# Performance work log

Measured on AMD Instinct MI355X. Metric: run time of the kernel, lower is better.

Reference implementation:

```python
import jax, jax.numpy as jnp
import numpy as np

N = 40000      # nodes
E = 640000     # edges (avg degree 16)
IN_DIM = 128
OUT_DIM = 128
HEADS = 4
NEG_SLOPE = 0.01  # torch F.leaky_relu default


def lrelu(x):
    return jnp.where(x >= 0, x, NEG_SLOPE * x)


def gat_layer(h, fc_W, attn_W, edge_w, m_w, src, dst, pd):
    """One GATLayer: z = lrelu(fc(h)); per-edge score; segment softmax over dst; weighted sum.
    fc_W: [D_out, D_in], attn_W: [1, 2*D_out], edge_w/m_w: [1,1] scalars, pd: [E,1]."""
    n = h.shape[0]
    z = lrelu(h @ fc_W.T)                      # [N, D]
    d = z.shape[1]
    # attn_fc(cat(z_src, z_dst)) = z_src@a_l + z_dst@a_r  (no bias)
    a_src = z @ attn_W[0, :d]                  # [N]
    a_dst = z @ attn_W[0, d:]                  # [N]
    a = a_src[src] + a_dst[dst]                # [E]
    ev = pd[:, 0] * edge_w[0, 0]               # edge_fc (Linear(1,1), no bias)
    e = lrelu(a * ev)                          # [E]
    ne = e * m_w[0, 0]                         # m_fc (Linear(1,1), no bias)
    # segment softmax over destination node (DGL mailbox softmax)
    m = jax.ops.segment_max(ne, dst, num_segments=n)
    m = jnp.where(jnp.isfinite(m), m, 0.0)     # empty mailboxes -> 0
    ex = jnp.exp(ne - m[dst])                  # [E]
    s = jax.ops.segment_sum(ex, dst, num_segments=n)
    denom = jnp.where(s > 0, s, 1.0)
    alpha = ex / denom[dst]                    # [E]
    # h_i = sum_j alpha_ij * z_j  (scatter-add over dst)
    return jax.ops.segment_sum(alpha[:, None] * z[src], dst, num_segments=n)


def gru_cell(x, hprev, Wih, Whh, bih, bhh):
    """torch.nn.GRUCell math. Wih/Whh: [3H, H]; gate order: reset, update, new."""
    gi = x @ Wih.T + bih
    gh = hprev @ Whh.T + bhh
    ir, iz, in_ = jnp.split(gi, 3, axis=1)
    hr, hz, hn = jnp.split(gh, 3, axis=1)
    r = jax.nn.sigmoid(ir + hr)
    zg = jax.nn.sigmoid(iz + hz)
    ng = jnp.tanh(in_ + r * hn)
    return (1.0 - zg) * ng + zg * hprev


def setup_inputs() -> dict:
    key = jax.random.key(0)
    ks = jax.random.split(key, 16)
    sc = 0.05
    inp = {
        "h": jax.random.normal(ks[0], (N, IN_DIM), jnp.float32),
        "pd": jax.random.uniform(ks[1], (E, 1), jnp.float32),
        "src": jax.random.randint(ks[2], (E,), 0, N, jnp.int32),
        "dst": jax.random.randint(ks[3], (E,), 0, N, jnp.int32),
        # per-head GATLayer params, stacked on leading head axis
        "fc_W": jax.random.normal(ks[4], (HEADS, OUT_DIM, IN_DIM), jnp.float32) * sc,
        "attn_W": jax.random.normal(ks[5], (HEADS, 1, 2 * OUT_DIM), jnp.float32) * sc,
        "edge_w": jax.random.normal(ks[6], (HEADS, 1, 1), jnp.float32) * sc + 1.0,
        "m_w": jax.random.normal(ks[7], (HEADS, 1, 1), jnp.float32) * sc + 1.0,
        # output GATLayer (in = HEADS*OUT_DIM)
        "out_fc_W": jax.random.normal(ks[8], (OUT_DIM, HEADS * OUT_DIM), jnp.float32) * sc,
        "out_attn_W": jax.random.normal(ks[9], (1, 2 * OUT_DIM), jnp.float32) * sc,
        "out_edge_w": jax.random.normal(ks[10], (1, 1), jnp.float32) * sc + 1.0,
        "out_m_w": jax.random.normal(ks[11], (1, 1), jnp.float32) * sc + 1.0,
        # GRUCell(OUT_DIM, OUT_DIM)
        "gru_Wih": jax.random.normal(ks[12], (3 * OUT_DIM, OUT_DIM), jnp.float32) * sc,
        "gru_Whh": jax.random.normal(ks[13], (3 * OUT_DIM, OUT_DIM), jnp.float32) * sc,
        "gru_bih": jax.random.normal(ks[14], (3 * OUT_DIM,), jnp.float32) * sc,
        "gru_bhh": jax.random.normal(ks[15], (3 * OUT_DIM,), jnp.float32) * sc,
    }
    return inp


def reference(h, pd, fc_W, attn_W, edge_w, m_w,
              out_fc_W, out_attn_W, out_edge_w, out_m_w,
              gru_Wih, gru_Whh, gru_bih, gru_bhh,
              src, dst):
    gru_in = h  # in_dim == out_dim -> no transform
    heads = [gat_layer(h, fc_W[i], attn_W[i], edge_w[i], m_w[i], src, dst, pd)
             for i in range(HEADS)]
    x = lrelu(jnp.concatenate(heads, axis=1))          # [N, HEADS*OUT_DIM]
    x = lrelu(gat_layer(x, out_fc_W, out_attn_W, out_edge_w, out_m_w, src, dst, pd))
    x = lrelu(gru_cell(x, gru_in, gru_Wih, gru_Whh, gru_bih, gru_bhh))
    return x
```

## Files before the change

### kernel.cpp

```cpp
#include <hip/hip_runtime.h>
#include <math.h>

#define NEG_SLOPE 0.01f

__device__ __forceinline__ float lrelu_f(float x) { return x >= 0.f ? x : NEG_SLOPE * x; }

typedef __attribute__((ext_vector_type(8))) short short8v;
typedef __attribute__((ext_vector_type(4))) short short4v;
typedef __attribute__((ext_vector_type(4))) float f32x4;
typedef __attribute__((ext_vector_type(8))) _Float16 half8v;
typedef __attribute__((ext_vector_type(4))) _Float16 half4v;

__device__ __forceinline__ unsigned short f2bf(float f) {
  unsigned u = __float_as_uint(f);
  u += 0x7FFF + ((u >> 16) & 1);
  return (unsigned short)(u >> 16);
}
__device__ __forceinline__ float bf2f(unsigned short s) {
  return __uint_as_float((unsigned)s << 16);
}

__global__ __launch_bounds__(256)
void split_bf16_k(const float* __restrict__ in, short* __restrict__ H,
                  short* __restrict__ L, int n4) {
  const int stride = gridDim.x * 256;
  for (int i = blockIdx.x * 256 + threadIdx.x; i < n4; i += stride) {
    const float4 v = ((const float4*)in)[i];
    short4v h, l;
    h[0] = (short)f2bf(v.x); l[0] = (short)f2bf(v.x - bf2f(h[0]));
    h[1] = (short)f2bf(v.y); l[1] = (short)f2bf(v.y - bf2f(h[1]));
    h[2] = (short)f2bf(v.z); l[2] = (short)f2bf(v.z - bf2f(h[2]));
    h[3] = (short)f2bf(v.w); l[3] = (short)f2bf(v.w - bf2f(h[3]));
    ((short4v*)H)[i] = h;
    ((short4v*)L)[i] = l;
  }
}

template<int TN, bool LRELU, bool BIAS, bool HOUT>
__global__ __launch_bounds__(256)
void gemm_bf16x3(const short* __restrict__ AH, const short* __restrict__ AL,
                 const short* __restrict__ BH, const short* __restrict__ BL,
                 const float* __restrict__ bias, float* __restrict__ C,
                 _Float16* __restrict__ Ch, int M, int Nn, int K) {
  constexpr int MI = (TN == 128) ? 4 : 2;
  constexpr int NI = 4;
  __shared__ short AsH[128 * 64], AsL[128 * 64];
  __shared__ short BsH[TN * 64],  BsL[TN * 64];
  const int tid = threadIdx.x;
  const int lane = tid & 63, w = tid >> 6;
  const int tx = tid & 15, ty = tid >> 4;
  const int bm = blockIdx.y << 7, bn = blockIdx.x * TN;
  const int m0 = (TN == 128) ? (w >> 1) * 64 : w * 32;
  const int n0 = (TN == 128) ? (w & 1) * 64 : 0;
  const int sbase = (tx >> 3) * 32 + (tx & 3) * 8 + ((tx >> 2) & 1) * 4;
  const int g = lane >> 4;
  const int key = (lane & 7) << 3;
  const int arow = lane & 15;

  f32x4 acc[MI][NI];
#pragma unroll
  for (int i = 0; i < MI; ++i)
#pragma unroll
    for (int j = 0; j < NI; ++j) acc[i][j] = (f32x4){0.f, 0.f, 0.f, 0.f};

  for (int k0 = 0; k0 < K; k0 += 64) {
#pragma unroll
    for (int i = 0; i < 8; ++i) {
      const int r = ty + (i << 4);
      int ar = bm + r; ar = ar < M ? ar : M - 1;
      const size_t go = (size_t)ar * K + k0 + (tx << 2);
      const short4v h = *(const short4v*)(AH + go);
      const short4v l = *(const short4v*)(AL + go);
      const int idx = r * 64 + (sbase ^ ((r & 7) << 3));
      *(short4v*)&AsH[idx] = h;
      *(short4v*)&AsL[idx] = l;
    }
#pragma unroll
    for (int i = 0; i < TN / 16; ++i) {
      const int r = ty + (i << 4);
      const size_t go = (size_t)(bn + r) * K + k0 + (tx << 2);
      const short4v h = *(const short4v*)(BH + go);
      const short4v l = *(const short4v*)(BL + go);
      const int idx = r * 64 + (sbase ^ ((r & 7) << 3));
      *(short4v*)&BsH[idx] = h;
      *(short4v*)&BsL[idx] = l;
    }
    __syncthreads();
#pragma unroll
    for (int kh = 0; kh < 2; ++kh) {
      const int sb = kh * 32 + g * 8;
      short8v aH[MI], aL[MI], bH[NI], bL[NI];
#pragma unroll
      for (int mi = 0; mi < MI; ++mi) {
        const int base = (m0 + arow + mi * 16) * 64 + (sb ^ key);
        aH[mi] = *(const short8v*)&AsH[base];
        aL[mi] = *(const short8v*)&AsL[base];
      }
#pragma unroll
      for (int ni = 0; ni < NI; ++ni) {
        const int base = (n0 + arow + ni * 16) * 64 + (sb ^ key);
        bH[ni] = *(const short8v*)&BsH[base];
        bL[ni] = *(const short8v*)&BsL[base];
      }
#pragma unroll
      for (int mi = 0; mi < MI; ++mi)
#pragma unroll
        for (int ni = 0; ni < NI; ++ni) {
          acc[mi][ni] = __builtin_amdgcn_mfma_f32_16x16x32_bf16(aH[mi], bH[ni], acc[mi][ni], 0, 0, 0);
          acc[mi][ni] = __builtin_amdgcn_mfma_f32_16x16x32_bf16(aH[mi], bL[ni], acc[mi][ni], 0, 0, 0);
          acc[mi][ni] = __builtin_amdgcn_mfma_f32_16x16x32_bf16(aL[mi], bH[ni], acc[mi][ni], 0, 0, 0);
        }
    }
    __syncthreads();
  }

  const int rg = (lane >> 4) << 2;
#pragma unroll
  for (int ni = 0; ni < NI; ++ni) {
    const int col = bn + n0 + ni * 16 + (lane & 15);
    const float bc = BIAS ? bias[col] : 0.f;
#pragma unroll
    for (int mi = 0; mi < MI; ++mi) {
#pragma unroll
      for (int r4 = 0; r4 < 4; ++r4) {
        const int row = bm + m0 + mi * 16 + rg + r4;
        if (row < M) {
          float v = acc[mi][ni][r4] + bc;
          if (LRELU) v = lrelu_f(v);
          C[(size_t)row * Nn + col] = v;
          if (HOUT) Ch[(size_t)row * Nn + col] = (_Float16)v;
        }
      }
    }
  }
}

__global__ __launch_bounds__(256)
void attn_heads_k(const float* __restrict__ z, const float* __restrict__ attnW,
                  float* __restrict__ asrc, float* __restrict__ adst, int N) {
  const int wid = (int)((blockIdx.x * (unsigned)blockDim.x + threadIdx.x) >> 6);
  const int lane = threadIdx.x & 63;
  if (wid >= N) return;
  const int h = lane >> 4;
  const int dd = (lane & 15) << 3;
  const float* zp = z + (size_t)wid * 512 + h * 128 + dd;
  const float* aw = attnW + h * 256 + dd;
  const float4 z0 = *(const float4*)zp;
  const float4 z1 = *(const float4*)(zp + 4);
  const float4 w0 = *(const float4*)aw;
  const float4 w1 = *(const float4*)(aw + 4);
  const float4 w2 = *(const float4*)(aw + 128);
  const float4 w3 = *(const float4*)(aw + 132);
  float ps = z0.x * w0.x + z0.y * w0.y + z0.z * w0.z + z0.w * w0.w
           + z1.x * w1.x + z1.y * w1.y + z1.z * w1.z + z1.w * w1.w;
  float pq = z0.x * w2.x + z0.y * w2.y + z0.z * w2.z + z0.w * w2.w
           + z1.x * w3.x + z1.y * w3.y + z1.z * w3.z + z1.w * w3.w;
#pragma unroll
  for (int off = 8; off; off >>= 1) {
    ps += __shfl_xor(ps, off);
    pq += __shfl_xor(pq, off);
  }
  if ((lane & 15) == 0) {
    asrc[(size_t)h * N + wid] = ps;
    adst[(size_t)h * N + wid] = pq;
  }
}

__global__ __launch_bounds__(256)
void attn_out_k(const float* __restrict__ z2, const float* __restrict__ attnW,
                float* __restrict__ asrc, float* __restrict__ adst, int N) {
  const int wid = (int)((blockIdx.x * (unsigned)blockDim.x + threadIdx.x) >> 6);
  const int lane = threadIdx.x & 63;
  if (wid >= N) return;
  const float* zp = z2 + (size_t)wid * 128;
  const float za = zp[lane], zb = zp[lane + 64];
  float ps = za * attnW[lane] + zb * attnW[lane + 64];
  float pq = za * attnW[128 + lane] + zb * attnW[192 + lane];
#pragma unroll
  for (int off = 32; off; off >>= 1) {
    ps += __shfl_xor(ps, off);
    pq += __shfl_xor(pq, off);
  }
  if (lane == 0) {
    asrc[wid] = ps;
    adst[wid] = pq;
  }
}

__global__ void hist_k(const int* __restrict__ dst, int* __restrict__ deg, int E) {
  const int i = blockIdx.x * 256 + threadIdx.x;
  if (i < E) atomicAdd(&deg[dst[i]], 1);
}

__global__ __launch_bounds__(1024)
void scan_k(const int* __restrict__ deg, int* __restrict__ ptr, int n) {
  __shared__ int wsum[16];
  __shared__ int carry_s;
  const int tid = threadIdx.x;
  const int lane = tid & 63, wv = tid >> 6;
  if (tid == 0) carry_s = 0;
  __syncthreads();
  for (int base = 0; base < n; base += 1024) {
    const int i = base + tid;
    int s = (i < n) ? deg[i] : 0;
#pragma unroll
    for (int off = 1; off < 64; off <<= 1) {
      const int t = __shfl_up(s, off);
      if (lane >= off) s += t;
    }
    if (lane == 63) wsum[wv] = s;
    __syncthreads();
    if (wv == 0 && lane < 16) {
      int ws = wsum[lane];
#pragma unroll
      for (int off = 1; off < 16; off <<= 1) {
        const int t = __shfl_up(ws, off);
        if (lane >= off) ws += t;
      }
      wsum[lane] = ws;
    }
    __syncthreads();
    const int wprefix = (wv == 0) ? 0 : wsum[wv - 1];
    const int carry = carry_s;
    if (i < n) ptr[i + 1] = carry + wprefix + s;
    __syncthreads();
    if (tid == 1023) carry_s = carry + wsum[15];
    __syncthreads();
  }
  if (tid == 0) ptr[0] = 0;
}

__global__ void scatter_k(const int* __restrict__ dst, const int* __restrict__ src,
                          const float* __restrict__ pd, const int* __restrict__ ptr,
                          int* __restrict__ cursor,
                          int* __restrict__ src_s, float* __restrict__ pd_s, int E) {
  const int i = blockIdx.x * 256 + threadIdx.x;
  if (i < E) {
    const int d = dst[i];
    const int p = ptr[d] + atomicAdd(&cursor[d], 1);
    src_s[p] = src[i];
    pd_s[p] = pd[i];
  }
}

__global__ __launch_bounds__(256)
void gat_heads_fused(const _Float16* __restrict__ zh,
                     const float* __restrict__ asrc, const float* __restrict__ adst,
                     const float* __restrict__ pd_s,
                     const float* __restrict__ ewp, const float* __restrict__ mwp,
                     const int* __restrict__ src_s, const int* __restrict__ csr_ptr,
                     float* __restrict__ outp, int N) {
  __shared__ float pair[4][128][5];
  const int wib = threadIdx.x >> 6;
  const int wid = blockIdx.x * 4 + wib;
  const int lane = threadIdx.x & 63;
  if (wid >= N) return;
  const int rs = csr_ptr[wid], re = csr_ptr[wid + 1];
  const int deg = re - rs;
  const int hh = lane >> 4;
  const int c = lane << 3;
  float* op = outp + (size_t)wid * 512 + c;
  if (deg == 0) {
    *(float4*)op = make_float4(0.f, 0.f, 0.f, 0.f);
    *(float4*)(op + 4) = make_float4(0.f, 0.f, 0.f, 0.f);
    return;
  }
  float ew[4], mwv[4], adn[4];
#pragma unroll
  for (int h = 0; h < 4; ++h) {
    ew[h] = ewp[h]; mwv[h] = mwp[h];
    adn[h] = adst[(size_t)h * N + wid];
  }
  const int j0 = rs + lane, j1 = j0 + 64;
  const bool v0 = j0 < re, v1 = j1 < re;
  const int s0 = v0 ? src_s[j0] : 0;
  const float p0 = v0 ? pd_s[j0] : 0.f;
  const int s1 = v1 ? src_s[j1] : 0;
  const float p1 = v1 ? pd_s[j1] : 0.f;
  float ne0[4], ne1[4], m[4];
#pragma unroll
  for (int h = 0; h < 4; ++h) {
    const float a0 = asrc[(size_t)h * N + s0];
    const float a1 = asrc[(size_t)h * N + s1];
    ne0[h] = v0 ? mwv[h] * lrelu_f((a0 + adn[h]) * (p0 * ew[h])) : -INFINITY;
    ne1[h] = v1 ? mwv[h] * lrelu_f((a1 + adn[h]) * (p1 * ew[h])) : -INFINITY;
    m[h] = fmaxf(ne0[h], ne1[h]);
  }
  for (int j = rs + 128 + lane; j < re; j += 64) {
    const int s = src_s[j];
    const float p = pd_s[j];
#pragma unroll
    for (int h = 0; h < 4; ++h)
      m[h] = fmaxf(m[h], mwv[h] * lrelu_f((asrc[(size_t)h * N + s] + adn[h]) * (p * ew[h])));
  }
#pragma unroll
  for (int h = 0; h < 4; ++h)
#pragma unroll
    for (int off = 32; off; off >>= 1) m[h] = fmaxf(m[h], __shfl_xor(m[h], off));

  float ss[4];
#pragma unroll
  for (int h = 0; h < 4; ++h) {
    const float e0 = expf(ne0[h] - m[h]);
    const float e1 = expf(ne1[h] - m[h]);
    pair[wib][lane][h] = e0;
    pair[wib][lane + 64][h] = e1;
    ss[h] = e0 + e1;
  }
  pair[wib][lane][4] = __int_as_float(s0);
  pair[wib][lane + 64][4] = __int_as_float(s1);
  for (int j = rs + 128 + lane; j < re; j += 64) {
    const int s = src_s[j];
    const float p = pd_s[j];
#pragma unroll
    for (int h = 0; h < 4; ++h)
      ss[h] += expf(mwv[h] * lrelu_f((asrc[(size_t)h * N + s] + adn[h]) * (p * ew[h])) - m[h]);
  }
#pragma unroll
  for (int h = 0; h < 4; ++h)
#pragma unroll
    for (int off = 32; off; off >>= 1) ss[h] += __shfl_xor(ss[h], off);

  float a[8] = {0.f, 0.f, 0.f, 0.f, 0.f, 0.f, 0.f, 0.f};
  for (int q0 = 0; q0 < deg; q0 += 2) {
#pragma unroll
    for (int u = 0; u < 2; ++u) {
      const int q = q0 + u;
      float exv; int sv;
      if (q < deg) {
        if (q < 128) {
          exv = pair[wib][q][hh];
          sv = __float_as_int(pair[wib][q][4]);
        } else {
          sv = src_s[rs + q];
          exv = expf(mwv[hh] * lrelu_f((asrc[(size_t)hh * N + sv] + adn[hh]) * (pd_s[rs + q] * ew[hh])) - m[hh]);
        }
      } else {
        exv = 0.f; sv = 0;
      }
      const half8v zv = *(const half8v*)(zh + (size_t)sv * 512 + c);
#pragma unroll
      for (int t = 0; t < 8; ++t) a[t] = fmaf(exv, (float)zv[t], a[t]);
    }
  }
  const float rd = 1.f / ((ss[hh] > 0.f) ? ss[hh] : 1.f);
  *(float4*)op = make_float4(lrelu_f(a[0] * rd), lrelu_f(a[1] * rd),
                             lrelu_f(a[2] * rd), lrelu_f(a[3] * rd));
  *(float4*)(op + 4) = make_float4(lrelu_f(a[4] * rd), lrelu_f(a[5] * rd),
                                   lrelu_f(a[6] * rd), lrelu_f(a[7] * rd));
}

__global__ __launch_bounds__(256)
void gat_out_aggregate(const _Float16* __restrict__ zh,
                       const float* __restrict__ asrc, const float* __restrict__ adst,
                       const float* __restrict__ pd_s,
                       const float* __restrict__ ewp, const float* __restrict__ mwp,
                       const int* __restrict__ src_s, const int* __restrict__ csr_ptr,
                       float* __restrict__ outp, int N) {
  __shared__ float pair[4][128][2];
  const int wib = threadIdx.x >> 6;
  const int wid = blockIdx.x * 4 + wib;
  const int lane = threadIdx.x & 63;
  if (wid >= N) return;
  const int rs = csr_ptr[wid], re = csr_ptr[wid + 1];
  const int deg = re - rs;
  const int l32 = lane & 31;
  const int half = lane >> 5;
  float* op = outp + (size_t)wid * 128;
  if (deg == 0) {
    if (half == 0) *(float4*)(op + (l32 << 2)) = make_float4(0.f, 0.f, 0.f, 0.f);
    return;
  }
  const float ew = ewp[0];
  const float mw = mwp[0];
  const float adn = adst[wid];

  float ne0 = -INFINITY, ne1 = -INFINITY;
  int s0 = 0, s1 = 0;
  {
    int j = rs + lane;
    if (j < re) {
      s0 = src_s[j];
      ne0 = mw * lrelu_f((asrc[s0] + adn) * (pd_s[j] * ew));
    }
    j += 64;
    if (j < re) {
      s1 = src_s[j];
      ne1 = mw * lrelu_f((asrc[s1] + adn) * (pd_s[j] * ew));
    }
  }
  float m = fmaxf(ne0, ne1);
  for (int j = rs + 128 + lane; j < re; j += 64) {
    const int s = src_s[j];
    m = fmaxf(m, mw * lrelu_f((asrc[s] + adn) * (pd_s[j] * ew)));
  }
#pragma unroll
  for (int off = 32; off; off >>= 1) m = fmaxf(m, __shfl_xor(m, off));

  const float ex0 = expf(ne0 - m);
  const float ex1 = expf(ne1 - m);
  float ss = ex0 + ex1;
  for (int j = rs + 128 + lane; j < re; j += 64) {
    const int s = src_s[j];
    ss += expf(mw * lrelu_f((asrc[s] + adn) * (pd_s[j] * ew)) - m);
  }
#pragma unroll
  for (int off = 32; off; off >>= 1) ss += __shfl_xor(ss, off);

  pair[wib][lane][0] = ex0;
  pair[wib][lane][1] = __int_as_float(s0);
  pair[wib][lane + 64][0] = ex1;
  pair[wib][lane + 64][1] = __int_as_float(s1);

  float a0 = 0.f, a1 = 0.f, a2 = 0.f, a3 = 0.f;
  const int zoff = l32 << 2;
  for (int q0 = 0; q0 < deg; q0 += 4) {
#pragma unroll
    for (int u = 0; u < 2; ++u) {
      const int q = q0 + (u << 1) + half;
      float exv; int sv;
      if (q < deg) {
        if (q < 128) {
          const float2 p = *(const float2*)&pair[wib][q][0];
          exv = p.x; sv = __float_as_int(p.y);
        } else {
          sv = src_s[rs + q];
          exv = expf(mw * lrelu_f((asrc[sv] + adn) * (pd_s[rs + q] * ew)) - m);
        }
      } else {
        exv = 0.f; sv = 0;
      }
      const half4v zv = *(const half4v*)(zh + (size_t)sv * 128 + zoff);
      a0 = fmaf(exv, (float)zv[0], a0);
      a1 = fmaf(exv, (float)zv[1], a1);
      a2 = fmaf(exv, (float)zv[2], a2);
      a3 = fmaf(exv, (float)zv[3], a3);
    }
  }
  a0 += __shfl_xor(a0, 32);
  a1 += __shfl_xor(a1, 32);
  a2 += __shfl_xor(a2, 32);
  a3 += __shfl_xor(a3, 32);
  if (half == 0) {
    const float rd = 1.f / ((ss > 0.f) ? ss : 1.f);
    *(float4*)(op + zoff) = make_float4(lrelu_f(a0 * rd), lrelu_f(a1 * rd),
                                        lrelu_f(a2 * rd), lrelu_f(a3 * rd));
  }
}

__global__ __launch_bounds__(256)
void gru_gate_k(const float* __restrict__ gi, const float* __restrict__ gh,
                const float* __restrict__ h, float* __restrict__ out, int total) {
  const int i = blockIdx.x * 256 + threadIdx.x;
  if (i >= total) return;
  const int n = i >> 7, d = i & 127;
  const float* gin = gi + (size_t)n * 384;
  const float* ghn = gh + (size_t)n * 384;
  const float r = 1.f / (1.f + expf(-(gin[d] + ghn[d])));
  const float zg = 1.f / (1.f + expf(-(gin[128 + d] + ghn[128 + d])));
  const float ng = tanhf(gin[256 + d] + r * ghn[256 + d]);
  const float v = (1.f - zg) * ng + zg * h[i];
  out[i] = lrelu_f(v);
}

extern "C" void kernel_launch(void* const* d_in, const int* in_sizes, int n_in,
                              void* d_out, int out_size, void* d_ws, size_t ws_size,
                              hipStream_t stream) {
  const int N = in_sizes[0] / 128;
  const int E = in_sizes[1];

  const float* h     = (const float*)d_in[0];
  const float* pd    = (const float*)d_in[1];
  const int*   src   = (const int*)d_in[2];
  const int*   dst   = (const int*)d_in[3];
  const float* fcW   = (const float*)d_in[4];
  const float* attnW = (const float*)d_in[5];
  const float* edgew = (const float*)d_in[6];
  const float* mw    = (const float*)d_in[7];
  const float* ofcW  = (const float*)d_in[8];
  const float* oattn = (const float*)d_in[9];
  const float* oew   = (const float*)d_in[10];
  const float* omw   = (const float*)d_in[11];
  const float* Wih   = (const float*)d_in[12];
  const float* Whh   = (const float*)d_in[13];
  const float* bih   = (const float*)d_in[14];
  const float* bhh   = (const float*)d_in[15];
  float* out = (float*)d_out;

  char* w = (char*)d_ws;
  size_t off = 0;
  auto alloc = [&](size_t bytes) -> char* {
    char* p = w + off;
    off += (bytes + 255) & ~(size_t)255;
    return p;
  };
  char* regA = alloc((size_t)N * 512 * 4);
  float* z   = (float*)regA;
  short* xH  = (short*)regA;
  short* xL  = (short*)(regA + (size_t)N * 512 * 2);
  float* gh  = (float*)regA;
  char* regB = alloc((size_t)N * 512 * 4);
  float* x   = (float*)regB;
  short* x2H = (short*)regB;
  short* x2L = (short*)(regB + (size_t)N * 128 * 2);
  float* gi  = (float*)(regB + (size_t)N * 128 * 4);
  _Float16* zh  = (_Float16*)alloc((size_t)N * 512 * 2);
  _Float16* z2h = (_Float16*)alloc((size_t)N * 128 * 2);
  float* z2    = (float*)alloc((size_t)N * 128 * 4);
  short* hH    = (short*)alloc((size_t)N * 128 * 2);
  short* hL    = (short*)alloc((size_t)N * 128 * 2);
  float* asrc  = (float*)alloc((size_t)4 * N * 4);
  float* adst  = (float*)alloc((size_t)4 * N * 4);
  float* a2s   = (float*)alloc((size_t)N * 4);
  float* a2d   = (float*)alloc((size_t)N * 4);
  int* deg     = (int*)alloc((size_t)N * 4);
  int* ptr     = (int*)alloc((size_t)(N + 1) * 4);
  int* cursor  = (int*)alloc((size_t)N * 4);
  int* src_s   = (int*)alloc((size_t)E * 4);
  float* pd_s  = (float*)alloc((size_t)E * 4);
  short* fcWH  = (short*)alloc((size_t)512 * 128 * 2);
  short* fcWL  = (short*)alloc((size_t)512 * 128 * 2);
  short* ofcWH = (short*)alloc((size_t)128 * 512 * 2);
  short* ofcWL = (short*)alloc((size_t)128 * 512 * 2);
  short* WihH  = (short*)alloc((size_t)384 * 128 * 2);
  short* WihL  = (short*)alloc((size_t)384 * 128 * 2);
  short* WhhH  = (short*)alloc((size_t)384 * 128 * 2);
  short* WhhL  = (short*)alloc((size_t)384 * 128 * 2);
  float* x2 = out;
  (void)ws_size; (void)n_in; (void)out_size;

  const int nodeBlocks = (N + 3) / 4;
  const int eBlocks = (E + 255) / 256;
  const int mBlocks = (N + 127) / 128;

  split_bf16_k<<<512, 256, 0, stream>>>(h, hH, hL, N * 128 / 4);
  split_bf16_k<<<64, 256, 0, stream>>>(fcW, fcWH, fcWL, 512 * 128 / 4);
  split_bf16_k<<<64, 256, 0, stream>>>(ofcW, ofcWH, ofcWL, 128 * 512 / 4);
  split_bf16_k<<<48, 256, 0, stream>>>(Wih, WihH, WihL, 384 * 128 / 4);
  split_bf16_k<<<48, 256, 0, stream>>>(Whh, WhhH, WhhL, 384 * 128 / 4);

  gemm_bf16x3<128, true, false, true><<<dim3(512 / 128, mBlocks), 256, 0, stream>>>(
      hH, hL, fcWH, fcWL, nullptr, z, zh, N, 512, 128);

  attn_heads_k<<<nodeBlocks, 256, 0, stream>>>(z, attnW, asrc, adst, N);

  hipMemsetAsync(deg, 0, (size_t)N * 4, stream);
  hipMemsetAsync(cursor, 0, (size_t)N * 4, stream);
  hist_k<<<eBlocks, 256, 0, stream>>>(dst, deg, E);
  scan_k<<<1, 1024, 0, stream>>>(deg, ptr, N);
  scatter_k<<<eBlocks, 256, 0, stream>>>(dst, src, pd, ptr, cursor, src_s, pd_s, E);

  gat_heads_fused<<<nodeBlocks, 256, 0, stream>>>(
      zh, asrc, adst, pd_s, edgew, mw, src_s, ptr, x, N);

  split_bf16_k<<<2048, 256, 0, stream>>>(x, xH, xL, N * 512 / 4);

  gemm_bf16x3<64, true, false, true><<<dim3(128 / 64, mBlocks), 256, 0, stream>>>(
      xH, xL, ofcWH, ofcWL, nullptr, z2, z2h, N, 128, 512);

  attn_out_k<<<nodeBlocks, 256, 0, stream>>>(z2, oattn, a2s, a2d, N);

  gat_out_aggregate<<<nodeBlocks, 256, 0, stream>>>(
      z2h, a2s, a2d, pd_s, oew, omw, src_s, ptr, x2, N);

  split_bf16_k<<<512, 256, 0, stream>>>(x2, x2H, x2L, N * 128 / 4);

  gemm_bf16x3<64, false, true, false><<<dim3(384 / 64, mBlocks), 256, 0, stream>>>(
      x2H, x2L, WihH, WihL, bih, gi, nullptr, N, 384, 128);
  gemm_bf16x3<64, false, true, false><<<dim3(384 / 64, mBlocks), 256, 0, stream>>>(
      hH, hL, WhhH, WhhL, bhh, gh, nullptr, N, 384, 128);

  gru_gate_k<<<(N * 128 + 255) / 256, 256, 0, stream>>>(gi, gh, h, out, N * 128);
}
```

Baseline: 612.4 us.

## Fuse bf16 hi/lo split into GAT aggregates and drop fp32 GEMM outputs

The two GAT aggregation kernels now write their results directly as bf16 high/low split pairs, which removes the two separate split_bf16 passes and their fp32 intermediate buffers. The first two GEMMs no longer store fp32 outputs, and the attention-score kernels read the fp16 copies instead, cutting global memory traffic. The aggregation loops are unrolled wider (4 or 8 neighbours per iteration) so more gathers are in flight at once. The cost is that the attention scores are now computed from fp16-rounded activations, which slightly changes the numerics.

```diff
diff --git a/kernel.cpp b/kernel.cpp
--- a/kernel.cpp
+++ b/kernel.cpp
@@ -36,7 +36,7 @@
   }
 }
 
-template<int TN, bool LRELU, bool BIAS, bool HOUT>
+template<int TN, bool LRELU, bool BIAS, bool COUT, bool HOUT>
 __global__ __launch_bounds__(256)
 void gemm_bf16x3(const short* __restrict__ AH, const short* __restrict__ AL,
                  const short* __restrict__ BH, const short* __restrict__ BL,
@@ -127,7 +127,7 @@
         if (row < M) {
           float v = acc[mi][ni][r4] + bc;
           if (LRELU) v = lrelu_f(v);
-          C[(size_t)row * Nn + col] = v;
+          if (COUT) C[(size_t)row * Nn + col] = v;
           if (HOUT) Ch[(size_t)row * Nn + col] = (_Float16)v;
         }
       }
@@ -136,25 +136,24 @@
 }
 
 __global__ __launch_bounds__(256)
-void attn_heads_k(const float* __restrict__ z, const float* __restrict__ attnW,
+void attn_heads_k(const _Float16* __restrict__ zh, const float* __restrict__ attnW,
                   float* __restrict__ asrc, float* __restrict__ adst, int N) {
   const int wid = (int)((blockIdx.x * (unsigned)blockDim.x + threadIdx.x) >> 6);
   const int lane = threadIdx.x & 63;
   if (wid >= N) return;
   const int h = lane >> 4;
   const int dd = (lane & 15) << 3;
-  const float* zp = z + (size_t)wid * 512 + h * 128 + dd;
+  const _Float16* zp = zh + (size_t)wid * 512 + h * 128 + dd;
   const float* aw = attnW + h * 256 + dd;
-  const float4 z0 = *(const float4*)zp;
-  const float4 z1 = *(const float4*)(zp + 4);
+  const half8v zv = *(const half8v*)zp;
   const float4 w0 = *(const float4*)aw;
   const float4 w1 = *(const float4*)(aw + 4);
   const float4 w2 = *(const float4*)(aw + 128);
   const float4 w3 = *(const float4*)(aw + 132);
-  float ps = z0.x * w0.x + z0.y * w0.y + z0.z * w0.z + z0.w * w0.w
-           + z1.x * w1.x + z1.y * w1.y + z1.z * w1.z + z1.w * w1.w;
-  float pq = z0.x * w2.x + z0.y * w2.y + z0.z * w2.z + z0.w * w2.w
-           + z1.x * w3.x + z1.y * w3.y + z1.z * w3.z + z1.w * w3.w;
+  float ps = (float)zv[0] * w0.x + (float)zv[1] * w0.y + (float)zv[2] * w0.z + (float)zv[3] * w0.w
+           + (float)zv[4] * w1.x + (float)zv[5] * w1.y + (float)zv[6] * w1.z + (float)zv[7] * w1.w;
+  float pq = (float)zv[0] * w2.x + (float)zv[1] * w2.y + (float)zv[2] * w2.z + (float)zv[3] * w2.w
+           + (float)zv[4] * w3.x + (float)zv[5] * w3.y + (float)zv[6] * w3.z + (float)zv[7] * w3.w;
 #pragma unroll
   for (int off = 8; off; off >>= 1) {
     ps += __shfl_xor(ps, off);
@@ -167,13 +166,13 @@
 }
 
 __global__ __launch_bounds__(256)
-void attn_out_k(const float* __restrict__ z2, const float* __restrict__ attnW,
+void attn_out_k(const _Float16* __restrict__ z2h, const float* __restrict__ attnW,
                 float* __restrict__ asrc, float* __restrict__ adst, int N) {
   const int wid = (int)((blockIdx.x * (unsigned)blockDim.x + threadIdx.x) >> 6);
   const int lane = threadIdx.x & 63;
   if (wid >= N) return;
-  const float* zp = z2 + (size_t)wid * 128;
-  const float za = zp[lane], zb = zp[lane + 64];
+  const _Float16* zp = z2h + (size_t)wid * 128;
+  const float za = (float)zp[lane], zb = (float)zp[lane + 64];
   float ps = za * attnW[lane] + zb * attnW[lane + 64];
   float pq = za * attnW[128 + lane] + zb * attnW[192 + lane];
 #pragma unroll
@@ -249,7 +248,7 @@
                      const float* __restrict__ pd_s,
                      const float* __restrict__ ewp, const float* __restrict__ mwp,
                      const int* __restrict__ src_s, const int* __restrict__ csr_ptr,
-                     float* __restrict__ outp, int N) {
+                     short* __restrict__ xH, short* __restrict__ xL, int N) {
   __shared__ float pair[4][128][5];
   const int wib = threadIdx.x >> 6;
   const int wid = blockIdx.x * 4 + wib;
@@ -259,10 +258,12 @@
   const int deg = re - rs;
   const int hh = lane >> 4;
   const int c = lane << 3;
-  float* op = outp + (size_t)wid * 512 + c;
+  short* opH = xH + (size_t)wid * 512 + c;
+  short* opL = xL + (size_t)wid * 512 + c;
   if (deg == 0) {
-    *(float4*)op = make_float4(0.f, 0.f, 0.f, 0.f);
-    *(float4*)(op + 4) = make_float4(0.f, 0.f, 0.f, 0.f);
+    short8v zv = {0, 0, 0, 0, 0, 0, 0, 0};
+    *(short8v*)opH = zv;
+    *(short8v*)opL = zv;
     return;
   }
   float ew[4], mwv[4], adn[4];
@@ -322,32 +323,42 @@
     for (int off = 32; off; off >>= 1) ss[h] += __shfl_xor(ss[h], off);
 
   float a[8] = {0.f, 0.f, 0.f, 0.f, 0.f, 0.f, 0.f, 0.f};
-  for (int q0 = 0; q0 < deg; q0 += 2) {
-#pragma unroll
-    for (int u = 0; u < 2; ++u) {
+  for (int q0 = 0; q0 < deg; q0 += 4) {
+    float exv[4]; int sv[4];
+#pragma unroll
+    for (int u = 0; u < 4; ++u) {
       const int q = q0 + u;
-      float exv; int sv;
       if (q < deg) {
         if (q < 128) {
-          exv = pair[wib][q][hh];
-          sv = __float_as_int(pair[wib][q][4]);
+          exv[u] = pair[wib][q][hh];
+          sv[u] = __float_as_int(pair[wib][q][4]);
         } else {
-          sv = src_s[rs + q];
-          exv = expf(mwv[hh] * lrelu_f((asrc[(size_t)hh * N + sv] + adn[hh]) * (pd_s[rs + q] * ew[hh])) - m[hh]);
+          sv[u] = src_s[rs + q];
+          exv[u] = expf(mwv[hh] * lrelu_f((asrc[(size_t)hh * N + sv[u]] + adn[hh]) * (pd_s[rs + q] * ew[hh])) - m[hh]);
         }
       } else {
-        exv = 0.f; sv = 0;
+        exv[u] = 0.f; sv[u] = 0;
       }
-      const half8v zv = *(const half8v*)(zh + (size_t)sv * 512 + c);
-#pragma unroll
-      for (int t = 0; t < 8; ++t) a[t] = fmaf(exv, (float)zv[t], a[t]);
-    }
+    }
+    half8v zv[4];
+#pragma unroll
+    for (int u = 0; u < 4; ++u)
+      zv[u] = *(const half8v*)(zh + (size_t)sv[u] * 512 + c);
+#pragma unroll
+    for (int u = 0; u < 4; ++u)
+#pragma unroll
+      for (int t = 0; t < 8; ++t) a[t] = fmaf(exv[u], (float)zv[u][t], a[t]);
   }
   const float rd = 1.f / ((ss[hh] > 0.f) ? ss[hh] : 1.f);
-  *(float4*)op = make_float4(lrelu_f(a[0] * rd), lrelu_f(a[1] * rd),
-                             lrelu_f(a[2] * rd), lrelu_f(a[3] * rd));
-  *(float4*)(op + 4) = make_float4(lrelu_f(a[4] * rd), lrelu_f(a[5] * rd),
-                                   lrelu_f(a[6] * rd), lrelu_f(a[7] * rd));
+  short8v hv, lv;
+#pragma unroll
+  for (int t = 0; t < 8; ++t) {
+    const float v = lrelu_f(a[t] * rd);
+    hv[t] = (short)f2bf(v);
+    lv[t] = (short)f2bf(v - bf2f((unsigned short)hv[t]));
+  }
+  *(short8v*)opH = hv;
+  *(short8v*)opL = lv;
 }
 
 __global__ __launch_bounds__(256)
@@ -356,7 +367,7 @@
                        const float* __restrict__ pd_s,
                        const float* __restrict__ ewp, const float* __restrict__ mwp,
                        const int* __restrict__ src_s, const int* __restrict__ csr_ptr,
-                       float* __restrict__ outp, int N) {
+                       short* __restrict__ x2H, short* __restrict__ x2L, int N) {
   __shared__ float pair[4][128][2];
   const int wib = threadIdx.x >> 6;
   const int wid = blockIdx.x * 4 + wib;
@@ -366,9 +377,15 @@
   const int deg = re - rs;
   const int l32 = lane & 31;
   const int half = lane >> 5;
-  float* op = outp + (size_t)wid * 128;
+  const int zoff = l32 << 2;
+  short* opH = x2H + (size_t)wid * 128 + zoff;
+  short* opL = x2L + (size_t)wid * 128 + zoff;
   if (deg == 0) {
-    if (half == 0) *(float4*)(op + (l32 << 2)) = make_float4(0.f, 0.f, 0.f, 0.f);
+    if (half == 0) {
+      short4v zv = {0, 0, 0, 0};
+      *(short4v*)opH = zv;
+      *(short4v*)opL = zv;
+    }
     return;
   }
   const float ew = ewp[0];
@@ -413,10 +430,9 @@
   pair[wib][lane + 64][1] = __int_as_float(s1);
 
   float a0 = 0.f, a1 = 0.f, a2 = 0.f, a3 = 0.f;
-  const int zoff = l32 << 2;
-  for (int q0 = 0; q0 < deg; q0 += 4) {
-#pragma unroll
-    for (int u = 0; u < 2; ++u) {
+  for (int q0 = 0; q0 < deg; q0 += 8) {
+#pragma unroll
+    for (int u = 0; u < 4; ++u) {
       const int q = q0 + (u << 1) + half;
       float exv; int sv;
       if (q < deg) {
@@ -443,8 +459,15 @@
   a3 += __shfl_xor(a3, 32);
   if (half == 0) {
     const float rd = 1.f / ((ss > 0.f) ? ss : 1.f);
-    *(float4*)(op + zoff) = make_float4(lrelu_f(a0 * rd), lrelu_f(a1 * rd),
-                                        lrelu_f(a2 * rd), lrelu_f(a3 * rd));
+    float v[4] = {lrelu_f(a0 * rd), lrelu_f(a1 * rd), lrelu_f(a2 * rd), lrelu_f(a3 * rd)};
+    short4v hv, lv;
+#pragma unroll
+    for (int t = 0; t < 4; ++t) {
+      hv[t] = (short)f2bf(v[t]);
+      lv[t] = (short)f2bf(v[t] - bf2f((unsigned short)hv[t]));
+    }
+    *(short4v*)opH = hv;
+    *(short4v*)opL = lv;
   }
 }
 
@@ -495,18 +518,15 @@
     return p;
   };
   char* regA = alloc((size_t)N * 512 * 4);
-  float* z   = (float*)regA;
   short* xH  = (short*)regA;
   short* xL  = (short*)(regA + (size_t)N * 512 * 2);
   float* gh  = (float*)regA;
   char* regB = alloc((size_t)N * 512 * 4);
-  float* x   = (float*)regB;
   short* x2H = (short*)regB;
   short* x2L = (short*)(regB + (size_t)N * 128 * 2);
   float* gi  = (float*)(regB + (size_t)N * 128 * 4);
   _Float16* zh  = (_Float16*)alloc((size_t)N * 512 * 2);
   _Float16* z2h = (_Float16*)alloc((size_t)N * 128 * 2);
-  float* z2    = (float*)alloc((size_t)N * 128 * 4);
   short* hH    = (short*)alloc((size_t)N * 128 * 2);
   short* hL    = (short*)alloc((size_t)N * 128 * 2);
   float* asrc  = (float*)alloc((size_t)4 * N * 4);
@@ -526,7 +546,6 @@
   short* WihL  = (short*)alloc((size_t)384 * 128 * 2);
   short* WhhH  = (short*)alloc((size_t)384 * 128 * 2);
   short* WhhL  = (short*)alloc((size_t)384 * 128 * 2);
-  float* x2 = out;
   (void)ws_size; (void)n_in; (void)out_size;
 
   const int nodeBlocks = (N + 3) / 4;
@@ -539,10 +558,10 @@
   split_bf16_k<<<48, 256, 0, stream>>>(Wih, WihH, WihL, 384 * 128 / 4);
   split_bf16_k<<<48, 256, 0, stream>>>(Whh, WhhH, WhhL, 384 * 128 / 4);
 
-  gemm_bf16x3<128, true, false, true><<<dim3(512 / 128, mBlocks), 256, 0, stream>>>(
-      hH, hL, fcWH, fcWL, nullptr, z, zh, N, 512, 128);
-
-  attn_heads_k<<<nodeBlocks, 256, 0, stream>>>(z, attnW, asrc, adst, N);
+  gemm_bf16x3<128, true, false, false, true><<<dim3(512 / 128, mBlocks), 256, 0, stream>>>(
+      hH, hL, fcWH, fcWL, nullptr, nullptr, zh, N, 512, 128);
+
+  attn_heads_k<<<nodeBlocks, 256, 0, stream>>>(zh, attnW, asrc, adst, N);
 
   hipMemsetAsync(deg, 0, (size_t)N * 4, stream);
   hipMemsetAsync(cursor, 0, (size_t)N * 4, stream);
@@ -551,23 +570,19 @@
   scatter_k<<<eBlocks, 256, 0, stream>>>(dst, src, pd, ptr, cursor, src_s, pd_s, E);
 
   gat_heads_fused<<<nodeBlocks, 256, 0, stream>>>(
-      zh, asrc, adst, pd_s, edgew, mw, src_s, ptr, x, N);
-
-  split_bf16_k<<<2048, 256, 0, stream>>>(x, xH, xL, N * 512 / 4);
-
-  gemm_bf16x3<64, true, false, true><<<dim3(128 / 64, mBlocks), 256, 0, stream>>>(
-      xH, xL, ofcWH, ofcWL, nullptr, z2, z2h, N, 128, 512);
-
-  attn_out_k<<<nodeBlocks, 256, 0, stream>>>(z2, oattn, a2s, a2d, N);
+      zh, asrc, adst, pd_s, edgew, mw, src_s, ptr, xH, xL, N);
+
+  gemm_bf16x3<64, true, false, false, true><<<dim3(128 / 64, mBlocks), 256, 0, stream>>>(
+      xH, xL, ofcWH, ofcWL, nullptr, nullptr, z2h, N, 128, 512);
+
+  attn_out_k<<<nodeBlocks, 256, 0, stream>>>(z2h, oattn, a2s, a2d, N);
 
   gat_out_aggregate<<<nodeBlocks, 256, 0, stream>>>(
-      z2h, a2s, a2d, pd_s, oew, omw, src_s, ptr, x2, N);
-
-  split_bf16_k<<<512, 256, 0, stream>>>(x2, x2H, x2L, N * 128 / 4);
-
-  gemm_bf16x3<64, false, true, false><<<dim3(384 / 64, mBlocks), 256, 0, stream>>>(
+      z2h, a2s, a2d, pd_s, oew, omw, src_s, ptr, x2H, x2L, N);
+
+  gemm_bf16x3<64, false, true, true, false><<<dim3(384 / 64, mBlocks), 256, 0, stream>>>(
       x2H, x2L, WihH, WihL, bih, gi, nullptr, N, 384, 128);
-  gemm_bf16x3<64, false, true, false><<<dim3(384 / 64, mBlocks), 256, 0, stream>>>(
+  gemm_bf16x3<64, false, true, true, false><<<dim3(384 / 64, mBlocks), 256, 0, stream>>>(
       hH, hL, WhhH, WhhL, bhh, gh, nullptr, N, 384, 128);
 
   gru_gate_k<<<(N * 128 + 255) / 256, 256, 0, stream>>>(gi, gh, h, out, N * 128);
```

New measurement: 558.4 us. 1.1x faster.
